# Performance work log

Measured on AMD Instinct MI355X. Metric: run time of the kernel, lower is better.

Reference implementation:

```python
import jax, jax.numpy as jnp
import numpy as np

RNN = 2048
NZ = 64
IN = 69  # 54 dofs + 15 actions


def gru_cell(x, h, w_ih, w_hh, b_ih, b_hh):
    gi = x @ w_ih.T + b_ih
    gh = h @ w_hh.T + b_hh
    i_r, i_z, i_n = jnp.split(gi, 3, axis=-1)
    h_r, h_z, h_n = jnp.split(gh, 3, axis=-1)
    r = jax.nn.sigmoid(i_r + h_r)
    z = jax.nn.sigmoid(i_z + h_z)
    n = jnp.tanh(i_n + r * h_n)
    return (1.0 - z) * n + z * h


def setup_inputs() -> dict:
    key = jax.random.key(0)
    ks = jax.random.split(key, 24)
    s = 0.02
    d = {
        'encoder_inputs': jax.random.normal(ks[0], (256, 49, IN), jnp.float32),
        'decoder_inputs': jax.random.normal(ks[1], (256, 25, IN), jnp.float32),
        'eps': jax.random.normal(ks[2], (256, NZ), jnp.float32),
        'fc0_w': jax.random.normal(ks[3], (RNN, 2 * IN), jnp.float32) * s,
        'fc0_b': jnp.zeros((RNN,), jnp.float32),
        'fc1_w': jax.random.normal(ks[4], (RNN, NZ + IN), jnp.float32) * s,
        'fc1_b': jnp.zeros((RNN,), jnp.float32),
        'fc2_w': jax.random.normal(ks[5], (IN, RNN), jnp.float32) * s,
        'fc2_b': jnp.zeros((IN,), jnp.float32),
        'mu_w': jax.random.normal(ks[6], (NZ, RNN), jnp.float32) * s,
        'mu_b': jnp.zeros((NZ,), jnp.float32),
        'sigma_w': jax.random.normal(ks[7], (NZ, RNN), jnp.float32) * s,
        'sigma_b': jnp.zeros((NZ,), jnp.float32),
        'c1_wih': jax.random.normal(ks[8], (3 * RNN, RNN), jnp.float32) * s,
        'c1_whh': jax.random.normal(ks[9], (3 * RNN, RNN), jnp.float32) * s,
        'c1_bih': jnp.zeros((3 * RNN,), jnp.float32),
        'c1_bhh': jnp.zeros((3 * RNN,), jnp.float32),
        'c2_wih': jax.random.normal(ks[10], (3 * RNN, IN), jnp.float32) * s,
        'c2_whh': jax.random.normal(ks[11], (3 * RNN, RNN), jnp.float32) * s,
        'c2_bih': jnp.zeros((3 * RNN,), jnp.float32),
        'c2_bhh': jnp.zeros((3 * RNN,), jnp.float32),
    }
    return d


def reference(encoder_inputs, decoder_inputs, eps, fc0_w, fc0_b, fc1_w, fc1_b, fc2_w, fc2_b,
              mu_w, mu_b, sigma_w, sigma_b, c1_wih, c1_whh, c1_bih, c1_bhh,
              c2_wih, c2_whh, c2_bih, c2_bhh):
    B = encoder_inputs.shape[0]
    enc_t = jnp.transpose(encoder_inputs, (1, 0, 2))  # [S-1, B, IN]
    dec_t = jnp.transpose(decoder_inputs, (1, 0, 2))  # [T, B, IN]
    # encoder step inputs: cat(enc[i], enc[i+1]); last step pairs with dec[0]
    nxt = jnp.concatenate([enc_t[1:], dec_t[:1]], axis=0)
    pairs = jnp.concatenate([enc_t, nxt], axis=-1)  # [S-1, B, 2*IN]
    x = pairs @ fc0_w.T + fc0_b  # fc0, [S-1, B, RNN]
    # precompute input-to-hidden GEMMs for all encoder steps
    gi_all = x @ c1_wih.T + c1_bih  # [S-1, B, 3*RNN]

    def enc_step(h, gi):
        gh = h @ c1_whh.T + c1_bhh
        i_r, i_z, i_n = jnp.split(gi, 3, axis=-1)
        h_r, h_z, h_n = jnp.split(gh, 3, axis=-1)
        r = jax.nn.sigmoid(i_r + h_r)
        z = jax.nn.sigmoid(i_z + h_z)
        n = jnp.tanh(i_n + r * h_n)
        return (1.0 - z) * n + z * h, None

    h0 = jnp.zeros((B, RNN), encoder_inputs.dtype)
    state, _ = jax.lax.scan(enc_step, h0, gi_all)

    z_mu = state @ mu_w.T + mu_b
    z_logvar = state @ sigma_w.T + sigma_b
    z = z_mu + eps * jnp.exp(0.5 * z_logvar)

    dec0 = dec_t[0]  # [B, IN]
    state = jnp.concatenate([z, dec0], axis=-1) @ fc1_w.T + fc1_b

    def dec_step(carry, _):
        h, inp = carry
        h = gru_cell(inp, h, c2_wih, c2_whh, c2_bih, c2_bhh)
        out = inp + (h @ fc2_w.T + fc2_b)  # residual feedback (eval: no dropout)
        return (h, out), out

    T = dec_t.shape[0]
    _, ys = jax.lax.scan(dec_step, (state, dec0), None, length=T)  # [T, B, IN]
    outputs = jnp.transpose(ys, (1, 0, 2))
    return outputs, z_mu, z_logvar
```

## Files before the change

kernel.cpp:

```cpp
#include <hip/hip_runtime.h>
#include <stdint.h>

#define B_    256
#define SE    49
#define TD    25
#define INDIM 69
#define RNN   2048
#define NZ    64
#define G3    6144

typedef __attribute__((ext_vector_type(8))) short short8_t;
typedef __attribute__((ext_vector_type(4))) float f32x4;
typedef unsigned short u16;

#define BARRIER() do { asm volatile("s_waitcnt lgkmcnt(0)" ::: "memory"); \
                       __builtin_amdgcn_s_barrier(); } while (0)

__device__ __forceinline__ u16 f2b(float f) {
  union { float f; unsigned u; } c; c.f = f;
  unsigned u = c.u;
  return (u16)((u + 0x7FFFu + ((u >> 16) & 1u)) >> 16);
}
__device__ __forceinline__ float sigm(float x) { return 1.f / (1.f + __expf(-x)); }
__device__ __forceinline__ short8_t ldbf(const u16* __restrict__ p, size_t off) {
  return *(const short8_t*)&p[off];
}

__device__ __forceinline__ int rmap(int R) {
  int bn = R / 96, rem = R % 96;
  int nw = rem / 48, g = (rem % 48) / 16, jj = rem % 16;
  return g * RNN + bn * 32 + nw * 16 + jj;
}

__global__ void k_reorder(const float* __restrict__ src, u16* __restrict__ dst, int K, int Kp) {
  int total = G3 * Kp;
  for (int i = blockIdx.x * blockDim.x + threadIdx.x; i < total; i += gridDim.x * blockDim.x) {
    int R = i / Kp, c = i % Kp;
    dst[i] = (c < K) ? f2b(src[(size_t)rmap(R) * K + c]) : (u16)0;
  }
}

__global__ void k_fc0T(const float* __restrict__ fc0w, const float* __restrict__ fc0b,
                       u16* __restrict__ dst) {
  int total = 256 * RNN;
  for (int i = blockIdx.x * blockDim.x + threadIdx.x; i < total; i += gridDim.x * blockDim.x) {
    int r = i >> 11, k = i & (RNN - 1);
    float v = 0.f;
    if (r < 2 * INDIM) v = fc0w[(size_t)k * (2 * INDIM) + r];
    else if (r == 2 * INDIM) v = fc0b[k];
    dst[i] = f2b(v);
  }
}

__global__ void k_fc2T(const float* __restrict__ fc2w, u16* __restrict__ dst) {
  int total = 96 * RNN;
  for (int i = blockIdx.x * blockDim.x + threadIdx.x; i < total; i += gridDim.x * blockDim.x) {
    int r = i >> 11, k = i & (RNN - 1);
    dst[i] = (r < INDIM) ? f2b(fc2w[(size_t)r * RNN + k]) : (u16)0;
  }
}

__global__ void k_pairs(const float* __restrict__ enc, const float* __restrict__ dec,
                        u16* __restrict__ pairs) {
  int total = SE * B_ * 256;
  for (int i = blockIdx.x * blockDim.x + threadIdx.x; i < total; i += gridDim.x * blockDim.x) {
    int c = i & 255, rb = i >> 8;
    int b = rb & 255, t = rb >> 8;
    float v = 0.f;
    if (c < INDIM) v = enc[((size_t)b * SE + t) * INDIM + c];
    else if (c < 2 * INDIM) {
      int cc = c - INDIM;
      v = (t < SE - 1) ? enc[((size_t)b * SE + t + 1) * INDIM + cc]
                       : dec[(size_t)b * TD * INDIM + cc];
    } else if (c == 2 * INDIM) v = 1.0f;
    pairs[i] = f2b(v);
  }
}

__global__ void k_msB(const float* __restrict__ muw, const float* __restrict__ sgw,
                      u16* __restrict__ dst) {
  int total = 128 * RNN;
  for (int i = blockIdx.x * blockDim.x + threadIdx.x; i < total; i += gridDim.x * blockDim.x) {
    int n = i >> 11, k = i & (RNN - 1);
    dst[i] = (n < NZ) ? f2b(muw[(size_t)n * RNN + k]) : f2b(sgw[(size_t)(n - NZ) * RNN + k]);
  }
}

__global__ void k_fc1B(const float* __restrict__ w, u16* __restrict__ dst) {
  int total = RNN * 192;
  for (int i = blockIdx.x * blockDim.x + threadIdx.x; i < total; i += gridDim.x * blockDim.x) {
    int n = i / 192, k = i % 192;
    dst[i] = (k < NZ + INDIM) ? f2b(w[(size_t)n * (NZ + INDIM) + k]) : (u16)0;
  }
}

__global__ void k_bias(const float* __restrict__ c1bih, const float* __restrict__ c1bhh,
                       const float* __restrict__ c2wih, const float* __restrict__ fc2b,
                       const float* __restrict__ c2bih, const float* __restrict__ c2bhh,
                       float* __restrict__ ebi, float* __restrict__ ebh,
                       float* __restrict__ dbi0, float* __restrict__ dbi1, float* __restrict__ dbh) {
  int R = blockIdx.x * blockDim.x + threadIdx.x;
  if (R >= G3) return;
  int orig = rmap(R);
  float k3 = 0.f;
  for (int o = 0; o < INDIM; ++o) k3 += c2wih[(size_t)orig * INDIM + o] * fc2b[o];
  ebi[R] = c1bih[orig];
  ebh[R] = c1bhh[orig];
  float d0 = c2bih[orig];
  dbi0[R] = d0;
  dbi1[R] = d0 + k3;
  dbh[R] = c2bhh[orig];
}

__global__ void k_init(float* __restrict__ hf, u16* __restrict__ hbf, float* __restrict__ fbuf,
                       float* __restrict__ omu, float* __restrict__ olv) {
  int i = blockIdx.x * blockDim.x + threadIdx.x;
  if (i < B_ * RNN) { hf[i] = 0.f; hbf[i] = 0; }
  if (i < 3 * B_ * 96) fbuf[i] = 0.f;
  if (i < B_ * NZ) { omu[i] = 0.f; olv[i] = 0.f; }
}

__global__ __launch_bounds__(256) void gemm_bt(
    const u16* __restrict__ A, const u16* __restrict__ W,
    u16* __restrict__ Cb, int N, int K)
{
  constexpr int BM = 128, BN = 128, BK = 64, LDK = BK + 8;
  __shared__ u16 sA[BM * LDK];
  __shared__ u16 sW[BN * LDK];
  const int ntn = N / BN;
  const int bm = blockIdx.x / ntn, bn = blockIdx.x % ntn;
  const int tid = threadIdx.x, lane = tid & 63, wave = tid >> 6;
  const int wr = wave >> 1, wc = wave & 1;
  f32x4 acc[4][4];
#pragma unroll
  for (int i = 0; i < 4; ++i)
#pragma unroll
    for (int j = 0; j < 4; ++j) acc[i][j] = (f32x4)(0.f);
  const int frow = lane & 15, fkq = (lane >> 4) * 8;
  for (int k0 = 0; k0 < K; k0 += BK) {
#pragma unroll
    for (int p = 0; p < 4; ++p) {
      int e = (p * 256 + tid) * 8, r = e / BK, c = e % BK;
      *(short8_t*)&sA[r * LDK + c] = *(const short8_t*)&A[(size_t)(bm * BM + r) * K + k0 + c];
    }
#pragma unroll
    for (int p = 0; p < 4; ++p) {
      int e = (p * 256 + tid) * 8, r = e / BK, c = e % BK;
      *(short8_t*)&sW[r * LDK + c] = *(const short8_t*)&W[(size_t)(bn * BN + r) * K + k0 + c];
    }
    __syncthreads();
#pragma unroll
    for (int kk = 0; kk < BK; kk += 32) {
      short8_t fa[4], fb[4];
#pragma unroll
      for (int m = 0; m < 4; ++m) fa[m] = *(const short8_t*)&sA[(wr * 64 + m * 16 + frow) * LDK + kk + fkq];
#pragma unroll
      for (int n = 0; n < 4; ++n) fb[n] = *(const short8_t*)&sW[(wc * 64 + n * 16 + frow) * LDK + kk + fkq];
#pragma unroll
      for (int m = 0; m < 4; ++m)
#pragma unroll
        for (int n = 0; n < 4; ++n)
          acc[m][n] = __builtin_amdgcn_mfma_f32_16x16x32_bf16(fa[m], fb[n], acc[m][n], 0, 0, 0);
    }
    __syncthreads();
  }
  const int crow = (lane >> 4) * 4, ccol = lane & 15;
#pragma unroll
  for (int n = 0; n < 4; ++n) {
    int col = bn * BN + wc * 64 + n * 16 + ccol;
#pragma unroll
    for (int m = 0; m < 4; ++m)
#pragma unroll
      for (int r = 0; r < 4; ++r) {
        int rowi = bm * BM + wr * 64 + m * 16 + crow + r;
        Cb[(size_t)rowi * N + col] = f2b(acc[m][n][r]);
      }
  }
}

struct Args {
  const u16 *pairs, *Wenc, *whh1, *whh2, *wih2, *fc2T;
  const u16 *msB, *fc1wB;
  const float *ebi, *ebh, *dbi0, *dbi1, *dbh;
  const float *eps, *dec, *fc1_b, *fc2_b, *mu_b, *sg_b;
  float* hf;
  u16*   hbf;
  float* fbuf;
  float* inp;
  u16*   inpbf;
  u16*   fc1xB;
  float *out, *out_mu, *out_lv;
};

__device__ __forceinline__ void compute_gi(const char* sA, const char* sW,
    f32x4 (&aR)[4], f32x4 (&aZ)[4], f32x4 (&aN)[4], int kg, int nw, int lane) {
#pragma unroll
  for (int s = 0; s < 2; ++s) {
    const int L = kg * 8 + s * 4 + (lane >> 4);
    short8_t fa[4], fb[3];
#pragma unroll
    for (int m = 0; m < 4; ++m) {
      int r = m * 16 + (lane & 15);
      fa[m] = *(const short8_t*)&sA[r * 512 + ((L ^ (r & 7)) * 16)];
    }
#pragma unroll
    for (int g = 0; g < 3; ++g) {
      int r = nw * 48 + g * 16 + (lane & 15);
      fb[g] = *(const short8_t*)&sW[r * 512 + ((L ^ (r & 7)) * 16)];
    }
#pragma unroll
    for (int m = 0; m < 4; ++m) {
      aR[m] = __builtin_amdgcn_mfma_f32_16x16x32_bf16(fa[m], fb[0], aR[m], 0, 0, 0);
      aZ[m] = __builtin_amdgcn_mfma_f32_16x16x32_bf16(fa[m], fb[1], aZ[m], 0, 0, 0);
      aN[m] = __builtin_amdgcn_mfma_f32_16x16x32_bf16(fa[m], fb[2], aN[m], 0, 0, 0);
    }
  }
}

__device__ __forceinline__ void compute_gh(const char* base,
    f32x4 (&aR)[4], f32x4 (&aZ)[4], f32x4 (&aN)[4], int kg, int nw, int lane) {
  const char* sA = base;
  const char* sW = base + 16384;
  const int L = kg * 4 + (lane >> 4);
  short8_t fa[4], fb[3];
#pragma unroll
  for (int m = 0; m < 4; ++m) {
    int r = m * 16 + (lane & 15);
    fa[m] = *(const short8_t*)&sA[r * 256 + ((L ^ (r & 15)) * 16)];
  }
#pragma unroll
  for (int g = 0; g < 3; ++g) {
    int r = nw * 48 + g * 16 + (lane & 15);
    fb[g] = *(const short8_t*)&sW[r * 256 + ((L ^ (r & 15)) * 16)];
  }
#pragma unroll
  for (int m = 0; m < 4; ++m) {
    aR[m] = __builtin_amdgcn_mfma_f32_16x16x32_bf16(fa[m], fb[0], aR[m], 0, 0, 0);
    aZ[m] = __builtin_amdgcn_mfma_f32_16x16x32_bf16(fa[m], fb[1], aZ[m], 0, 0, 0);
    aN[m] = __builtin_amdgcn_mfma_f32_16x16x32_bf16(fa[m], fb[2], aN[m], 0, 0, 0);
  }
}

__device__ __forceinline__ void reduce_and_gate(
    f32x4 (&aR)[4], f32x4 (&aZ)[4], f32x4 (&aNI)[4], f32x4 (&aNH)[4],
    char* smem, int tid, int bm, int bn,
    const float* __restrict__ bi, const float* __restrict__ bh,
    const float* __restrict__ hfold, float* __restrict__ hfnew, u16* __restrict__ hbnew) {
  const int lane = tid & 63, wid = tid >> 6;
  auto wr16 = [&](int slots, int w) {
#pragma unroll
    for (int m = 0; m < 4; ++m) {
      *(f32x4*)&smem[(((0 * 4 + m) * slots + w) * 64 + lane) * 16] = aR[m];
      *(f32x4*)&smem[(((1 * 4 + m) * slots + w) * 64 + lane) * 16] = aZ[m];
      *(f32x4*)&smem[(((2 * 4 + m) * slots + w) * 64 + lane) * 16] = aNI[m];
      *(f32x4*)&smem[(((3 * 4 + m) * slots + w) * 64 + lane) * 16] = aNH[m];
    }
  };
  auto add16 = [&](int slots, int w) {
#pragma unroll
    for (int m = 0; m < 4; ++m) {
      aR[m]  += *(const f32x4*)&smem[(((0 * 4 + m) * slots + w) * 64 + lane) * 16];
      aZ[m]  += *(const f32x4*)&smem[(((1 * 4 + m) * slots + w) * 64 + lane) * 16];
      aNI[m] += *(const f32x4*)&smem[(((2 * 4 + m) * slots + w) * 64 + lane) * 16];
      aNH[m] += *(const f32x4*)&smem[(((3 * 4 + m) * slots + w) * 64 + lane) * 16];
    }
  };
  __syncthreads();
  if (wid >= 4) wr16(4, wid - 4);
  __syncthreads();
  if (wid < 4) add16(4, wid);
  __syncthreads();
  if (wid == 2 || wid == 3) wr16(2, wid - 2);
  __syncthreads();
  if (wid < 2) {
    add16(2, wid);
    const int nw = wid, jj = lane & 15;
    const int Rb = bn * 96 + nw * 48;
    const float biR = bi[Rb + jj],      bhR = bh[Rb + jj];
    const float biZ = bi[Rb + 16 + jj], bhZ = bh[Rb + 16 + jj];
    const float biN = bi[Rb + 32 + jj], bhN = bh[Rb + 32 + jj];
    const int j = bn * 32 + nw * 16 + jj;
#pragma unroll
    for (int m = 0; m < 4; ++m)
#pragma unroll
      for (int q = 0; q < 4; ++q) {
        int b = bm * 64 + m * 16 + ((lane >> 4) << 2) + q;
        float r = sigm(aR[m][q] + biR + bhR);
        float z = sigm(aZ[m][q] + biZ + bhZ);
        float nn = 2.f * sigm(2.f * ((aNI[m][q] + biN) + r * (aNH[m][q] + bhN))) - 1.f;
        float hv = (1.f - z) * nn + z * hfold[(size_t)b * RNN + j];
        hfnew[(size_t)b * RNN + j] = hv;
        hbnew[(size_t)b * RNN + j] = f2b(hv);
      }
  }
}

__global__ __launch_bounds__(512, 1) void k_enc(Args a, int t) {
  __shared__ char smem[81920];
  const int tid = threadIdx.x, lane = tid & 63, wid = tid >> 6;
  const int kg = wid >> 1, nw = wid & 1;
  const int bm = blockIdx.x >> 6, bn = blockIdx.x & 63;
  const int rowA0 = bm * 64, rowW0 = bn * 96;
  const int pin = t & 1, pout = pin ^ 1;
  const u16* hin = a.hbf + (size_t)pin * B_ * RNN;
  const float* hfold = a.hf + (size_t)pin * B_ * RNN;
  float* hfnew = a.hf + (size_t)pout * B_ * RNN;
  u16* hbnew = a.hbf + (size_t)pout * B_ * RNN;
  const int sr32 = tid >> 5, sc32 = tid & 31;
  const int sr16 = tid >> 4, sc16 = tid & 15;

  f32x4 aR[4], aZ[4], aNI[4], aNH[4];
#pragma unroll
  for (int m = 0; m < 4; ++m) {
    aR[m] = (f32x4)(0.f); aZ[m] = (f32x4)(0.f);
    aNI[m] = (f32x4)(0.f); aNH[m] = (f32x4)(0.f);
  }

  auto issue_gh = [&](short8_t (&ra)[2], short8_t (&rw)[3], int k0) {
#pragma unroll
    for (int p = 0; p < 2; ++p) {
      int r = p * 32 + sr16;
      ra[p] = ldbf(hin, (size_t)(rowA0 + r) * RNN + k0 + sc16 * 8);
    }
#pragma unroll
    for (int p = 0; p < 3; ++p) {
      int r = p * 32 + sr16;
      rw[p] = ldbf(a.whh1, (size_t)(rowW0 + r) * RNN + k0 + sc16 * 8);
    }
  };
  auto write_gh = [&](char* base, short8_t (&ra)[2], short8_t (&rw)[3]) {
#pragma unroll
    for (int p = 0; p < 2; ++p) {
      int r = p * 32 + sr16;
      *(short8_t*)&base[r * 256 + ((sc16 ^ (r & 15)) * 16)] = ra[p];
    }
#pragma unroll
    for (int p = 0; p < 3; ++p) {
      int r = p * 32 + sr16;
      *(short8_t*)&(base + 16384)[r * 256 + ((sc16 ^ (r & 15)) * 16)] = rw[p];
    }
  };

  {
    const u16* P = a.pairs + (size_t)t * B_ * 256;
    short8_t ga[4], gw[6];
#pragma unroll
    for (int p = 0; p < 4; ++p) {
      int r = p * 16 + sr32;
      ga[p] = ldbf(P, (size_t)(rowA0 + r) * 256 + sc32 * 8);
    }
#pragma unroll
    for (int p = 0; p < 6; ++p) {
      int r = p * 16 + sr32;
      gw[p] = ldbf(a.Wenc, (size_t)(rowW0 + r) * 256 + sc32 * 8);
    }
#pragma unroll
    for (int p = 0; p < 4; ++p) {
      int r = p * 16 + sr32;
      *(short8_t*)&smem[r * 512 + ((sc32 ^ (r & 7)) * 16)] = ga[p];
    }
#pragma unroll
    for (int p = 0; p < 6; ++p) {
      int r = p * 16 + sr32;
      *(short8_t*)&smem[32768 + r * 512 + ((sc32 ^ (r & 7)) * 16)] = gw[p];
    }
  }
  short8_t rA0[2], rW0[3], rA1[2], rW1[3];
  issue_gh(rA0, rW0, 0);
  issue_gh(rA1, rW1, 128);
  BARRIER();
  compute_gi(smem, smem + 32768, aR, aZ, aNI, kg, nw, lane);
  BARRIER();
  write_gh(smem, rA0, rW0);
  issue_gh(rA0, rW0, 2 * 128);
  BARRIER();
#pragma unroll
  for (int i = 0; i < 16; ++i) {
    char* cb = (i & 1) ? smem + 40960 : smem;
    if (i + 1 <= 15) {
      char* nb = ((i + 1) & 1) ? smem + 40960 : smem;
      if ((i + 1) & 1) {
        write_gh(nb, rA1, rW1);
        if (i + 3 <= 15) issue_gh(rA1, rW1, (i + 3) * 128);
      } else {
        write_gh(nb, rA0, rW0);
        if (i + 3 <= 15) issue_gh(rA0, rW0, (i + 3) * 128);
      }
    }
    compute_gh(cb, aR, aZ, aNH, kg, nw, lane);
    if (i < 15) BARRIER();
  }
  reduce_and_gate(aR, aZ, aNI, aNH, smem, tid, bm, bn, a.ebi, a.ebh, hfold, hfnew, hbnew);
}

__global__ __launch_bounds__(512, 1) void k_dec(Args a, int t) {
  __shared__ char smem[81920];
  const int tid = threadIdx.x, lane = tid & 63, wid = tid >> 6;
  const int kg = wid >> 1, nw = wid & 1;
  const int bm = blockIdx.x >> 6, bn = blockIdx.x & 63;
  const int rowA0 = bm * 64, rowW0 = bn * 96;
  const int pin = t & 1, pout = pin ^ 1;
  const int irs = (t + 1) & 1, iws = t & 1;
  const int frd = (t + 2) % 3;
  const u16* hin = a.hbf + (size_t)pin * B_ * RNN;
  const float* hfold = a.hf + (size_t)pin * B_ * RNN;
  float* hfnew = a.hf + (size_t)pout * B_ * RNN;
  u16* hbnew = a.hbf + (size_t)pout * B_ * RNN;
  const int gtid = blockIdx.x * 512 + tid;
  const int sr32 = tid >> 5, sc32 = tid & 31;
  const int sr16 = tid >> 4, sc16 = tid & 15;
  const int fr = lane & 15, fq = (lane >> 4) << 3;

  if (t >= 1 && gtid < B_ * INDIM) {
    int b = gtid / INDIM, o = gtid % INDIM;
    float v = a.inp[(size_t)irs * B_ * INDIM + gtid] +
              a.fbuf[(size_t)frd * B_ * 96 + b * 96 + o] + a.fc2_b[o];
    a.out[((size_t)b * TD + (t - 1)) * INDIM + o] = v;
    a.inp[(size_t)iws * B_ * INDIM + gtid] = v;
    a.inpbf[(size_t)iws * B_ * 128 + b * 128 + o] = f2b(v);
  }
  if (gtid < B_ * 96)
    a.fbuf[(size_t)((t + 1) % 3) * B_ * 96 + gtid] = 0.f;

  f32x4 aR[4], aZ[4], aNI[4], aNH[4];
#pragma unroll
  for (int m = 0; m < 4; ++m) {
    aR[m] = (f32x4)(0.f); aZ[m] = (f32x4)(0.f);
    aNI[m] = (f32x4)(0.f); aNH[m] = (f32x4)(0.f);
  }

  auto issue_gh = [&](short8_t (&ra)[2], short8_t (&rw)[3], int k0) {
#pragma unroll
    for (int p = 0; p < 2; ++p) {
      int r = p * 32 + sr16;
      ra[p] = ldbf(hin, (size_t)(rowA0 + r) * RNN + k0 + sc16 * 8);
    }
#pragma unroll
    for (int p = 0; p < 3; ++p) {
      int r = p * 32 + sr16;
      rw[p] = ldbf(a.whh2, (size_t)(rowW0 + r) * RNN + k0 + sc16 * 8);
    }
  };
  auto write_gh = [&](char* base, short8_t (&ra)[2], short8_t (&rw)[3]) {
#pragma unroll
    for (int p = 0; p < 2; ++p) {
      int r = p * 32 + sr16;
      *(short8_t*)&base[r * 256 + ((sc16 ^ (r & 15)) * 16)] = ra[p];
    }
#pragma unroll
    for (int p = 0; p < 3; ++p) {
      int r = p * 32 + sr16;
      *(short8_t*)&(base + 16384)[r * 256 + ((sc16 ^ (r & 15)) * 16)] = rw[p];
    }
  };

  {
    const u16* inpA = a.inpbf + (size_t)irs * B_ * 128;
    const float* F = a.fbuf + (size_t)frd * B_ * 96;
    short8_t ga[4], gw[6];
#pragma unroll
    for (int p = 0; p < 4; ++p) {
      int r = p * 16 + sr32;
      if (sc32 < 16) {
        ga[p] = ldbf(inpA, (size_t)(rowA0 + r) * 128 + sc32 * 8);
      } else {
        short8_t v;
        int o0 = (sc32 - 16) * 8;
#pragma unroll
        for (int e = 0; e < 8; ++e) {
          int o = o0 + e;
          float fv = (o < 96) ? F[(size_t)(rowA0 + r) * 96 + o] : 0.f;
          v[e] = (short)f2b(fv);
        }
        ga[p] = v;
      }
    }
#pragma unroll
    for (int p = 0; p < 6; ++p) {
      int r = p * 16 + sr32;
      gw[p] = ldbf(a.wih2, (size_t)(rowW0 + r) * 128 + (sc32 & 15) * 8);
    }
#pragma unroll
    for (int p = 0; p < 4; ++p) {
      int r = p * 16 + sr32;
      *(short8_t*)&smem[r * 512 + ((sc32 ^ (r & 7)) * 16)] = ga[p];
    }
#pragma unroll
    for (int p = 0; p < 6; ++p) {
      int r = p * 16 + sr32;
      *(short8_t*)&smem[32768 + r * 512 + ((sc32 ^ (r & 7)) * 16)] = gw[p];
    }
  }
  short8_t rA0[2], rW0[3], rA1[2], rW1[3];
  issue_gh(rA0, rW0, 0);
  issue_gh(rA1, rW1, 128);
  BARRIER();
  compute_gi(smem, smem + 32768, aR, aZ, aNI, kg, nw, lane);
  BARRIER();
  write_gh(smem, rA0, rW0);
  issue_gh(rA0, rW0, 2 * 128);
  BARRIER();
#pragma unroll
  for (int i = 0; i < 16; ++i) {
    char* cb = (i & 1) ? smem + 40960 : smem;
    if (i + 1 <= 15) {
      char* nb = ((i + 1) & 1) ? smem + 40960 : smem;
      if ((i + 1) & 1) {
        write_gh(nb, rA1, rW1);
        if (i + 3 <= 15) issue_gh(rA1, rW1, (i + 3) * 128);
      } else {
        write_gh(nb, rA0, rW0);
        if (i + 3 <= 15) issue_gh(rA0, rW0, (i + 3) * 128);
      }
    }
    compute_gh(cb, aR, aZ, aNH, kg, nw, lane);
    if (i < 15) BARRIER();
  }
  reduce_and_gate(aR, aZ, aNI, aNH, smem, tid, bm, bn,
                  (t >= 1) ? a.dbi1 : a.dbi0, a.dbh, hfold, hfnew, hbnew);

  __syncthreads();
  if (wid < 4) {
    const int wr = wid >> 1, wc = wid & 1;
    const int kcol = bn * 32 + fq;
    short8_t fa[2], fb[3];
#pragma unroll
    for (int m = 0; m < 2; ++m)
      fa[m] = ldbf(hbnew, (size_t)(bm * 64 + wr * 32 + m * 16 + fr) * RNN + kcol);
#pragma unroll
    for (int n = 0; n < 3; ++n)
      fb[n] = ldbf(a.fc2T, (size_t)(wc * 48 + n * 16 + fr) * RNN + kcol);
    f32x4 accf[2][3];
#pragma unroll
    for (int m = 0; m < 2; ++m)
#pragma unroll
      for (int n = 0; n < 3; ++n) accf[m][n] = (f32x4)(0.f);
#pragma unroll
    for (int m = 0; m < 2; ++m)
#pragma unroll
      for (int n = 0; n < 3; ++n)
        accf[m][n] = __builtin_amdgcn_mfma_f32_16x16x32_bf16(fa[m], fb[n], accf[m][n], 0, 0, 0);
    float* fdst = a.fbuf + (size_t)(t % 3) * B_ * 96;
#pragma unroll
    for (int m = 0; m < 2; ++m)
#pragma unroll
      for (int n = 0; n < 3; ++n)
#pragma unroll
        for (int q = 0; q < 4; ++q) {
          int row = bm * 64 + wr * 32 + m * 16 + ((lane >> 4) << 2) + q;
          int col = wc * 48 + n * 16 + (lane & 15);
          atomicAdd(&fdst[row * 96 + col], accf[m][n][q]);
        }
  }
}

__global__ __launch_bounds__(256) void k_msm(Args a) {
  const int bm = blockIdx.x >> 3, kc = blockIdx.x & 7;
  const int lane = threadIdx.x & 63, wid = threadIdx.x >> 6;
  const int wr = wid >> 1, wc = wid & 1;
  const int fr = lane & 15, fq = (lane >> 4) << 3;
  const u16* h1 = a.hbf + (size_t)B_ * RNN;
  f32x4 acc[4][4];
#pragma unroll
  for (int m = 0; m < 4; ++m)
#pragma unroll
    for (int n = 0; n < 4; ++n) acc[m][n] = (f32x4)(0.f);
#pragma unroll
  for (int ks = 0; ks < 8; ++ks) {
    const int k = kc * 256 + ks * 32 + fq;
    short8_t fa[4], fb[4];
#pragma unroll
    for (int m = 0; m < 4; ++m)
      fa[m] = ldbf(h1, (size_t)(bm * 128 + wr * 64 + m * 16 + fr) * RNN + k);
#pragma unroll
    for (int n = 0; n < 4; ++n)
      fb[n] = ldbf(a.msB, (size_t)(wc * 64 + n * 16 + fr) * RNN + k);
#pragma unroll
    for (int m = 0; m < 4; ++m)
#pragma unroll
      for (int n = 0; n < 4; ++n)
        acc[m][n] = __builtin_amdgcn_mfma_f32_16x16x32_bf16(fa[m], fb[n], acc[m][n], 0, 0, 0);
  }
#pragma unroll
  for (int m = 0; m < 4; ++m)
#pragma unroll
    for (int n = 0; n < 4; ++n)
#pragma unroll
      for (int q = 0; q < 4; ++q) {
        int row = bm * 128 + wr * 64 + m * 16 + ((lane >> 4) << 2) + q;
        int col = wc * 64 + n * 16 + (lane & 15);
        if (col < NZ) atomicAdd(&a.out_mu[row * NZ + col], acc[m][n][q]);
        else          atomicAdd(&a.out_lv[row * NZ + col - NZ], acc[m][n][q]);
      }
}

__global__ void k_sample(Args a) {
  int gid = blockIdx.x * blockDim.x + threadIdx.x;
  if (gid < B_ * NZ) {
    int b = gid >> 6, n = gid & 63;
    float mu = a.out_mu[gid] + a.mu_b[n];
    float lv = a.out_lv[gid] + a.sg_b[n];
    a.out_mu[gid] = mu;
    a.out_lv[gid] = lv;
    a.fc1xB[b * 192 + n] = f2b(mu + a.eps[gid] * __expf(0.5f * lv));
  }
  if (gid < B_ * 128) {
    int b = gid >> 7, c = gid & 127;
    float v = (c < INDIM) ? a.dec[(size_t)b * TD * INDIM + c] : 0.f;
    u16 vb = f2b(v);
    a.inpbf[(size_t)b * 128 + c] = vb;
    a.inpbf[(size_t)B_ * 128 + b * 128 + c] = vb;
    if (c < INDIM) {
      a.inp[b * INDIM + c] = v;
      a.inp[B_ * INDIM + b * INDIM + c] = v;
      a.fc1xB[b * 192 + NZ + c] = f2b(v);
    }
  }
  if (gid < B_ * 192) {
    int c = gid % 192;
    if (c >= NZ + INDIM) a.fc1xB[gid] = 0;
  }
}

__global__ __launch_bounds__(256) void k_fc1m(Args a) {
  const int bm = blockIdx.x >> 4, bn = blockIdx.x & 15;
  const int lane = threadIdx.x & 63, wid = threadIdx.x >> 6;
  const int wr = wid >> 1, wc = wid & 1;
  const int fr = lane & 15, fq = (lane >> 4) << 3;
  f32x4 acc[4][4];
#pragma unroll
  for (int m = 0; m < 4; ++m)
#pragma unroll
    for (int n = 0; n < 4; ++n) acc[m][n] = (f32x4)(0.f);
#pragma unroll
  for (int ks = 0; ks < 6; ++ks) {
    const int k = ks * 32 + fq;
    short8_t fa[4], fb[4];
#pragma unroll
    for (int m = 0; m < 4; ++m)
      fa[m] = ldbf(a.fc1xB, (size_t)(bm * 128 + wr * 64 + m * 16 + fr) * 192 + k);
#pragma unroll
    for (int n = 0; n < 4; ++n)
      fb[n] = ldbf(a.fc1wB, (size_t)(bn * 128 + wc * 64 + n * 16 + fr) * 192 + k);
#pragma unroll
    for (int m = 0; m < 4; ++m)
#pragma unroll
      for (int n = 0; n < 4; ++n)
        acc[m][n] = __builtin_amdgcn_mfma_f32_16x16x32_bf16(fa[m], fb[n], acc[m][n], 0, 0, 0);
  }
#pragma unroll
  for (int n = 0; n < 4; ++n) {
    const int col = bn * 128 + wc * 64 + n * 16 + (lane & 15);
    const float bv = a.fc1_b[col];
#pragma unroll
    for (int m = 0; m < 4; ++m)
#pragma unroll
      for (int q = 0; q < 4; ++q) {
        int row = bm * 128 + wr * 64 + m * 16 + ((lane >> 4) << 2) + q;
        float v = acc[m][n][q] + bv;
        a.hf[(size_t)row * RNN + col] = v;
        a.hbf[(size_t)row * RNN + col] = f2b(v);
      }
  }
}

__global__ void k_tail(Args a) {
  int i = blockIdx.x * blockDim.x + threadIdx.x;
  if (i < B_ * INDIM) {
    int b = i / INDIM, o = i % INDIM;
    float v = a.inp[(size_t)(24 & 1) * B_ * INDIM + i] +
              a.fbuf[(size_t)(24 % 3) * B_ * 96 + b * 96 + o] + a.fc2_b[o];
    a.out[((size_t)b * TD + 24) * INDIM + o] = v;
  }
}

extern "C" void kernel_launch(void* const* d_in, const int* in_sizes, int n_in,
                              void* d_out, int out_size, void* d_ws, size_t ws_size,
                              hipStream_t stream)
{
  const float* enc    = (const float*)d_in[0];
  const float* dec    = (const float*)d_in[1];
  const float* eps    = (const float*)d_in[2];
  const float* fc0_w  = (const float*)d_in[3];
  const float* fc0_b  = (const float*)d_in[4];
  const float* fc1_w  = (const float*)d_in[5];
  const float* fc1_b  = (const float*)d_in[6];
  const float* fc2_w  = (const float*)d_in[7];
  const float* fc2_b  = (const float*)d_in[8];
  const float* mu_w   = (const float*)d_in[9];
  const float* mu_b   = (const float*)d_in[10];
  const float* sg_w   = (const float*)d_in[11];
  const float* sg_b   = (const float*)d_in[12];
  const float* c1_wih = (const float*)d_in[13];
  const float* c1_whh = (const float*)d_in[14];
  const float* c1_bih = (const float*)d_in[15];
  const float* c1_bhh = (const float*)d_in[16];
  const float* c2_wih = (const float*)d_in[17];
  const float* c2_whh = (const float*)d_in[18];
  const float* c2_bih = (const float*)d_in[19];
  const float* c2_bhh = (const float*)d_in[20];

  float* out_outputs = (float*)d_out;
  float* out_mu = out_outputs + (size_t)B_ * TD * INDIM;
  float* out_lv = out_mu + (size_t)B_ * NZ;

  char* ws = (char*)d_ws;
  size_t off = 0;
  auto alloc = [&](size_t bytes) -> void* {
    void* p = ws + off; off += (bytes + 255) & ~(size_t)255; return p;
  };

  u16* whh1_r = (u16*)alloc((size_t)G3 * RNN * 2);
  u16* whh2_r = (u16*)alloc((size_t)G3 * RNN * 2);
  u16* wih1_r = (u16*)alloc((size_t)G3 * RNN * 2);
  u16* wih2_r = (u16*)alloc((size_t)G3 * 128 * 2);
  u16* fc0T   = (u16*)alloc((size_t)256 * RNN * 2);
  u16* fc2T   = (u16*)alloc((size_t)96 * RNN * 2);
  u16* Wenc   = (u16*)alloc((size_t)G3 * 256 * 2);
  u16* pairs  = (u16*)alloc((size_t)SE * B_ * 256 * 2);
  u16* msB    = (u16*)alloc((size_t)128 * RNN * 2);
  u16* fc1wB  = (u16*)alloc((size_t)RNN * 192 * 2);
  float* hf   = (float*)alloc((size_t)2 * B_ * RNN * 4);
  u16* hbf    = (u16*)alloc((size_t)2 * B_ * RNN * 2);
  float* fbuf = (float*)alloc((size_t)3 * B_ * 96 * 4);
  float* inp  = (float*)alloc((size_t)2 * B_ * INDIM * 4);
  u16* inpbf  = (u16*)alloc((size_t)2 * B_ * 128 * 2);
  u16* fc1xB  = (u16*)alloc((size_t)B_ * 192 * 2);
  float* ebi  = (float*)alloc((size_t)G3 * 4);
  float* ebh  = (float*)alloc((size_t)G3 * 4);
  float* dbi0 = (float*)alloc((size_t)G3 * 4);
  float* dbi1 = (float*)alloc((size_t)G3 * 4);
  float* dbh  = (float*)alloc((size_t)G3 * 4);
  (void)ws_size; (void)in_sizes; (void)n_in; (void)out_size;

  k_reorder<<<4096, 256, 0, stream>>>(c1_whh, whh1_r, RNN, RNN);
  k_reorder<<<4096, 256, 0, stream>>>(c2_whh, whh2_r, RNN, RNN);
  k_reorder<<<4096, 256, 0, stream>>>(c1_wih, wih1_r, RNN, RNN);
  k_reorder<<<1024, 256, 0, stream>>>(c2_wih, wih2_r, INDIM, 128);
  k_fc0T<<<512, 256, 0, stream>>>(fc0_w, fc0_b, fc0T);
  k_fc2T<<<256, 256, 0, stream>>>(fc2_w, fc2T);
  k_pairs<<<2048, 256, 0, stream>>>(enc, dec, pairs);
  k_msB<<<256, 256, 0, stream>>>(mu_w, sg_w, msB);
  k_fc1B<<<256, 256, 0, stream>>>(fc1_w, fc1wB);
  k_bias<<<24, 256, 0, stream>>>(c1_bih, c1_bhh, c2_wih, fc2_b, c2_bih, c2_bhh,
                                 ebi, ebh, dbi0, dbi1, dbh);

  Args a;
  a.pairs = pairs; a.Wenc = Wenc; a.whh1 = whh1_r; a.whh2 = whh2_r;
  a.wih2 = wih2_r; a.fc2T = fc2T; a.msB = msB; a.fc1wB = fc1wB;
  a.ebi = ebi; a.ebh = ebh; a.dbi0 = dbi0; a.dbi1 = dbi1; a.dbh = dbh;
  a.eps = eps; a.dec = dec; a.fc1_b = fc1_b; a.fc2_b = fc2_b;
  a.mu_b = mu_b; a.sg_b = sg_b;
  a.hf = hf; a.hbf = hbf; a.fbuf = fbuf; a.inp = inp; a.inpbf = inpbf;
  a.fc1xB = fc1xB; a.out = out_outputs; a.out_mu = out_mu; a.out_lv = out_lv;

  k_init<<<2048, 256, 0, stream>>>(hf, hbf, fbuf, out_mu, out_lv);
  gemm_bt<<<(G3 / 128) * (256 / 128), 256, 0, stream>>>(wih1_r, fc0T, Wenc, 256, RNN);

  for (int t = 0; t < SE; ++t)
    k_enc<<<256, 512, 0, stream>>>(a, t);
  k_msm<<<16, 256, 0, stream>>>(a);
  k_sample<<<192, 256, 0, stream>>>(a);
  k_fc1m<<<32, 256, 0, stream>>>(a);
  for (int t = 0; t < TD; ++t)
    k_dec<<<256, 512, 0, stream>>>(a, t);
  k_tail<<<69, 256, 0, stream>>>(a);
}
```

Baseline: 1.435 ms.

## Fuse per-step GRU launches into persistent cooperative kernels with grid sync

Replaces the 49 encoder and 25 decoder per-timestep kernel launches with one cooperative kernel each. The kernel loops over timesteps and uses a cooperative-groups grid barrier between steps, falling back to per-step launches if the cooperative launch fails. This removes launch overhead and the kernel-boundary drain between dependent steps. In exchange it adds a grid-wide sync cost and relies on all 256 blocks being co-resident. The decoder also relies on memory ordering across the grid barrier for the fbuf atomics and the inp handoff.

```diff
diff --git a/kernel.cpp b/kernel.cpp
--- a/kernel.cpp
+++ b/kernel.cpp
@@ -1,5 +1,8 @@
 #include <hip/hip_runtime.h>
+#include <hip/hip_cooperative_groups.h>
 #include <stdint.h>
+
+namespace cg = cooperative_groups;
 
 #define B_    256
 #define SE    49
@@ -247,7 +250,7 @@
     const float* __restrict__ bi, const float* __restrict__ bh,
     const float* __restrict__ hfold, float* __restrict__ hfnew, u16* __restrict__ hbnew) {
   const int lane = tid & 63, wid = tid >> 6;
-  auto wr16 = [&](int slots, int w) {
+  auto wrp = [&](int slots, int w) {
 #pragma unroll
     for (int m = 0; m < 4; ++m) {
       *(f32x4*)&smem[(((0 * 4 + m) * slots + w) * 64 + lane) * 16] = aR[m];
@@ -256,7 +259,7 @@
       *(f32x4*)&smem[(((3 * 4 + m) * slots + w) * 64 + lane) * 16] = aNH[m];
     }
   };
-  auto add16 = [&](int slots, int w) {
+  auto addp = [&](int slots, int w) {
 #pragma unroll
     for (int m = 0; m < 4; ++m) {
       aR[m]  += *(const f32x4*)&smem[(((0 * 4 + m) * slots + w) * 64 + lane) * 16];
@@ -266,14 +269,14 @@
     }
   };
   __syncthreads();
-  if (wid >= 4) wr16(4, wid - 4);
+  if (wid >= 4) wrp(4, wid - 4);
   __syncthreads();
-  if (wid < 4) add16(4, wid);
+  if (wid < 4) addp(4, wid);
   __syncthreads();
-  if (wid == 2 || wid == 3) wr16(2, wid - 2);
+  if (wid == 2 || wid == 3) wrp(2, wid - 2);
   __syncthreads();
   if (wid < 2) {
-    add16(2, wid);
+    addp(2, wid);
     const int nw = wid, jj = lane & 15;
     const int Rb = bn * 96 + nw * 48;
     const float biR = bi[Rb + jj],      bhR = bh[Rb + jj];
@@ -295,262 +298,274 @@
   }
 }
 
-__global__ __launch_bounds__(512, 1) void k_enc(Args a, int t) {
+template<int COOP>
+__global__ __launch_bounds__(512, 1) void k_enc_run(Args a, int t0, int nsteps) {
   __shared__ char smem[81920];
   const int tid = threadIdx.x, lane = tid & 63, wid = tid >> 6;
   const int kg = wid >> 1, nw = wid & 1;
   const int bm = blockIdx.x >> 6, bn = blockIdx.x & 63;
   const int rowA0 = bm * 64, rowW0 = bn * 96;
-  const int pin = t & 1, pout = pin ^ 1;
-  const u16* hin = a.hbf + (size_t)pin * B_ * RNN;
-  const float* hfold = a.hf + (size_t)pin * B_ * RNN;
-  float* hfnew = a.hf + (size_t)pout * B_ * RNN;
-  u16* hbnew = a.hbf + (size_t)pout * B_ * RNN;
   const int sr32 = tid >> 5, sc32 = tid & 31;
   const int sr16 = tid >> 4, sc16 = tid & 15;
 
-  f32x4 aR[4], aZ[4], aNI[4], aNH[4];
-#pragma unroll
-  for (int m = 0; m < 4; ++m) {
-    aR[m] = (f32x4)(0.f); aZ[m] = (f32x4)(0.f);
-    aNI[m] = (f32x4)(0.f); aNH[m] = (f32x4)(0.f);
-  }
-
-  auto issue_gh = [&](short8_t (&ra)[2], short8_t (&rw)[3], int k0) {
-#pragma unroll
-    for (int p = 0; p < 2; ++p) {
-      int r = p * 32 + sr16;
-      ra[p] = ldbf(hin, (size_t)(rowA0 + r) * RNN + k0 + sc16 * 8);
-    }
-#pragma unroll
-    for (int p = 0; p < 3; ++p) {
-      int r = p * 32 + sr16;
-      rw[p] = ldbf(a.whh1, (size_t)(rowW0 + r) * RNN + k0 + sc16 * 8);
-    }
-  };
-  auto write_gh = [&](char* base, short8_t (&ra)[2], short8_t (&rw)[3]) {
-#pragma unroll
-    for (int p = 0; p < 2; ++p) {
-      int r = p * 32 + sr16;
-      *(short8_t*)&base[r * 256 + ((sc16 ^ (r & 15)) * 16)] = ra[p];
-    }
-#pragma unroll
-    for (int p = 0; p < 3; ++p) {
-      int r = p * 32 + sr16;
-      *(short8_t*)&(base + 16384)[r * 256 + ((sc16 ^ (r & 15)) * 16)] = rw[p];
-    }
-  };
-
-  {
-    const u16* P = a.pairs + (size_t)t * B_ * 256;
-    short8_t ga[4], gw[6];
-#pragma unroll
-    for (int p = 0; p < 4; ++p) {
-      int r = p * 16 + sr32;
-      ga[p] = ldbf(P, (size_t)(rowA0 + r) * 256 + sc32 * 8);
-    }
-#pragma unroll
-    for (int p = 0; p < 6; ++p) {
-      int r = p * 16 + sr32;
-      gw[p] = ldbf(a.Wenc, (size_t)(rowW0 + r) * 256 + sc32 * 8);
-    }
-#pragma unroll
-    for (int p = 0; p < 4; ++p) {
-      int r = p * 16 + sr32;
-      *(short8_t*)&smem[r * 512 + ((sc32 ^ (r & 7)) * 16)] = ga[p];
-    }
-#pragma unroll
-    for (int p = 0; p < 6; ++p) {
-      int r = p * 16 + sr32;
-      *(short8_t*)&smem[32768 + r * 512 + ((sc32 ^ (r & 7)) * 16)] = gw[p];
-    }
-  }
-  short8_t rA0[2], rW0[3], rA1[2], rW1[3];
-  issue_gh(rA0, rW0, 0);
-  issue_gh(rA1, rW1, 128);
-  BARRIER();
-  compute_gi(smem, smem + 32768, aR, aZ, aNI, kg, nw, lane);
-  BARRIER();
-  write_gh(smem, rA0, rW0);
-  issue_gh(rA0, rW0, 2 * 128);
-  BARRIER();
-#pragma unroll
-  for (int i = 0; i < 16; ++i) {
-    char* cb = (i & 1) ? smem + 40960 : smem;
-    if (i + 1 <= 15) {
-      char* nb = ((i + 1) & 1) ? smem + 40960 : smem;
-      if ((i + 1) & 1) {
-        write_gh(nb, rA1, rW1);
-        if (i + 3 <= 15) issue_gh(rA1, rW1, (i + 3) * 128);
-      } else {
-        write_gh(nb, rA0, rW0);
-        if (i + 3 <= 15) issue_gh(rA0, rW0, (i + 3) * 128);
-      }
-    }
-    compute_gh(cb, aR, aZ, aNH, kg, nw, lane);
-    if (i < 15) BARRIER();
-  }
-  reduce_and_gate(aR, aZ, aNI, aNH, smem, tid, bm, bn, a.ebi, a.ebh, hfold, hfnew, hbnew);
-}
-
-__global__ __launch_bounds__(512, 1) void k_dec(Args a, int t) {
+  for (int t = t0; t < t0 + nsteps; ++t) {
+    const int pin = t & 1, pout = pin ^ 1;
+    const u16* hin = a.hbf + (size_t)pin * B_ * RNN;
+    const float* hfold = a.hf + (size_t)pin * B_ * RNN;
+    float* hfnew = a.hf + (size_t)pout * B_ * RNN;
+    u16* hbnew = a.hbf + (size_t)pout * B_ * RNN;
+
+    f32x4 aR[4], aZ[4], aNI[4], aNH[4];
+#pragma unroll
+    for (int m = 0; m < 4; ++m) {
+      aR[m] = (f32x4)(0.f); aZ[m] = (f32x4)(0.f);
+      aNI[m] = (f32x4)(0.f); aNH[m] = (f32x4)(0.f);
+    }
+
+    auto issue_gh = [&](short8_t (&ra)[2], short8_t (&rw)[3], int k0) {
+#pragma unroll
+      for (int p = 0; p < 2; ++p) {
+        int r = p * 32 + sr16;
+        ra[p] = ldbf(hin, (size_t)(rowA0 + r) * RNN + k0 + sc16 * 8);
+      }
+#pragma unroll
+      for (int p = 0; p < 3; ++p) {
+        int r = p * 32 + sr16;
+        rw[p] = ldbf(a.whh1, (size_t)(rowW0 + r) * RNN + k0 + sc16 * 8);
+      }
+    };
+    auto write_gh = [&](char* base, short8_t (&ra)[2], short8_t (&rw)[3]) {
+#pragma unroll
+      for (int p = 0; p < 2; ++p) {
+        int r = p * 32 + sr16;
+        *(short8_t*)&base[r * 256 + ((sc16 ^ (r & 15)) * 16)] = ra[p];
+      }
+#pragma unroll
+      for (int p = 0; p < 3; ++p) {
+        int r = p * 32 + sr16;
+        *(short8_t*)&(base + 16384)[r * 256 + ((sc16 ^ (r & 15)) * 16)] = rw[p];
+      }
+    };
+
+    {
+      const u16* P = a.pairs + (size_t)t * B_ * 256;
+      short8_t ga[4], gw[6];
+#pragma unroll
+      for (int p = 0; p < 4; ++p) {
+        int r = p * 16 + sr32;
+        ga[p] = ldbf(P, (size_t)(rowA0 + r) * 256 + sc32 * 8);
+      }
+#pragma unroll
+      for (int p = 0; p < 6; ++p) {
+        int r = p * 16 + sr32;
+        gw[p] = ldbf(a.Wenc, (size_t)(rowW0 + r) * 256 + sc32 * 8);
+      }
+#pragma unroll
+      for (int p = 0; p < 4; ++p) {
+        int r = p * 16 + sr32;
+        *(short8_t*)&smem[r * 512 + ((sc32 ^ (r & 7)) * 16)] = ga[p];
+      }
+#pragma unroll
+      for (int p = 0; p < 6; ++p) {
+        int r = p * 16 + sr32;
+        *(short8_t*)&(smem + 32768)[r * 512 + ((sc32 ^ (r & 7)) * 16)] = gw[p];
+      }
+    }
+    short8_t rA0[2], rW0[3], rA1[2], rW1[3];
+    issue_gh(rA0, rW0, 0);
+    issue_gh(rA1, rW1, 128);
+    BARRIER();
+    compute_gi(smem, smem + 32768, aR, aZ, aNI, kg, nw, lane);
+    BARRIER();
+    write_gh(smem, rA0, rW0);
+    issue_gh(rA0, rW0, 2 * 128);
+    BARRIER();
+#pragma unroll
+    for (int i = 0; i < 16; ++i) {
+      char* cb = (i & 1) ? smem + 40960 : smem;
+      if (i + 1 <= 15) {
+        char* nb = ((i + 1) & 1) ? smem + 40960 : smem;
+        if ((i + 1) & 1) {
+          write_gh(nb, rA1, rW1);
+          if (i + 3 <= 15) issue_gh(rA1, rW1, (i + 3) * 128);
+        } else {
+          write_gh(nb, rA0, rW0);
+          if (i + 3 <= 15) issue_gh(rA0, rW0, (i + 3) * 128);
+        }
+      }
+      compute_gh(cb, aR, aZ, aNH, kg, nw, lane);
+      if (i < 15) BARRIER();
+    }
+    reduce_and_gate(aR, aZ, aNI, aNH, smem, tid, bm, bn, a.ebi, a.ebh, hfold, hfnew, hbnew);
+
+    if (COOP && t + 1 < t0 + nsteps) cg::this_grid().sync();
+  }
+}
+
+template<int COOP>
+__global__ __launch_bounds__(512, 1) void k_dec_run(Args a, int t0, int nsteps) {
   __shared__ char smem[81920];
   const int tid = threadIdx.x, lane = tid & 63, wid = tid >> 6;
   const int kg = wid >> 1, nw = wid & 1;
   const int bm = blockIdx.x >> 6, bn = blockIdx.x & 63;
   const int rowA0 = bm * 64, rowW0 = bn * 96;
-  const int pin = t & 1, pout = pin ^ 1;
-  const int irs = (t + 1) & 1, iws = t & 1;
-  const int frd = (t + 2) % 3;
-  const u16* hin = a.hbf + (size_t)pin * B_ * RNN;
-  const float* hfold = a.hf + (size_t)pin * B_ * RNN;
-  float* hfnew = a.hf + (size_t)pout * B_ * RNN;
-  u16* hbnew = a.hbf + (size_t)pout * B_ * RNN;
-  const int gtid = blockIdx.x * 512 + tid;
   const int sr32 = tid >> 5, sc32 = tid & 31;
   const int sr16 = tid >> 4, sc16 = tid & 15;
   const int fr = lane & 15, fq = (lane >> 4) << 3;
-
-  if (t >= 1 && gtid < B_ * INDIM) {
-    int b = gtid / INDIM, o = gtid % INDIM;
-    float v = a.inp[(size_t)irs * B_ * INDIM + gtid] +
-              a.fbuf[(size_t)frd * B_ * 96 + b * 96 + o] + a.fc2_b[o];
-    a.out[((size_t)b * TD + (t - 1)) * INDIM + o] = v;
-    a.inp[(size_t)iws * B_ * INDIM + gtid] = v;
-    a.inpbf[(size_t)iws * B_ * 128 + b * 128 + o] = f2b(v);
-  }
-  if (gtid < B_ * 96)
-    a.fbuf[(size_t)((t + 1) % 3) * B_ * 96 + gtid] = 0.f;
-
-  f32x4 aR[4], aZ[4], aNI[4], aNH[4];
-#pragma unroll
-  for (int m = 0; m < 4; ++m) {
-    aR[m] = (f32x4)(0.f); aZ[m] = (f32x4)(0.f);
-    aNI[m] = (f32x4)(0.f); aNH[m] = (f32x4)(0.f);
-  }
-
-  auto issue_gh = [&](short8_t (&ra)[2], short8_t (&rw)[3], int k0) {
-#pragma unroll
-    for (int p = 0; p < 2; ++p) {
-      int r = p * 32 + sr16;
-      ra[p] = ldbf(hin, (size_t)(rowA0 + r) * RNN + k0 + sc16 * 8);
-    }
-#pragma unroll
-    for (int p = 0; p < 3; ++p) {
-      int r = p * 32 + sr16;
-      rw[p] = ldbf(a.whh2, (size_t)(rowW0 + r) * RNN + k0 + sc16 * 8);
-    }
-  };
-  auto write_gh = [&](char* base, short8_t (&ra)[2], short8_t (&rw)[3]) {
-#pragma unroll
-    for (int p = 0; p < 2; ++p) {
-      int r = p * 32 + sr16;
-      *(short8_t*)&base[r * 256 + ((sc16 ^ (r & 15)) * 16)] = ra[p];
-    }
-#pragma unroll
-    for (int p = 0; p < 3; ++p) {
-      int r = p * 32 + sr16;
-      *(short8_t*)&(base + 16384)[r * 256 + ((sc16 ^ (r & 15)) * 16)] = rw[p];
-    }
-  };
-
-  {
-    const u16* inpA = a.inpbf + (size_t)irs * B_ * 128;
-    const float* F = a.fbuf + (size_t)frd * B_ * 96;
-    short8_t ga[4], gw[6];
-#pragma unroll
-    for (int p = 0; p < 4; ++p) {
-      int r = p * 16 + sr32;
-      if (sc32 < 16) {
-        ga[p] = ldbf(inpA, (size_t)(rowA0 + r) * 128 + sc32 * 8);
-      } else {
-        short8_t v;
-        int o0 = (sc32 - 16) * 8;
-#pragma unroll
-        for (int e = 0; e < 8; ++e) {
-          int o = o0 + e;
-          float fv = (o < 96) ? F[(size_t)(rowA0 + r) * 96 + o] : 0.f;
-          v[e] = (short)f2b(fv);
+  const int gtid = blockIdx.x * 512 + tid;
+
+  for (int t = t0; t < t0 + nsteps; ++t) {
+    const int pin = t & 1, pout = pin ^ 1;
+    const int irs = (t + 1) & 1, iws = t & 1;
+    const int frd = (t + 2) % 3;
+    const u16* hin = a.hbf + (size_t)pin * B_ * RNN;
+    const float* hfold = a.hf + (size_t)pin * B_ * RNN;
+    float* hfnew = a.hf + (size_t)pout * B_ * RNN;
+    u16* hbnew = a.hbf + (size_t)pout * B_ * RNN;
+
+    if (t >= 1 && gtid < B_ * INDIM) {
+      int b = gtid / INDIM, o = gtid % INDIM;
+      float v = a.inp[(size_t)irs * B_ * INDIM + gtid] +
+                a.fbuf[(size_t)frd * B_ * 96 + b * 96 + o] + a.fc2_b[o];
+      a.out[((size_t)b * TD + (t - 1)) * INDIM + o] = v;
+      a.inp[(size_t)iws * B_ * INDIM + gtid] = v;
+      a.inpbf[(size_t)iws * B_ * 128 + b * 128 + o] = f2b(v);
+    }
+    if (gtid < B_ * 96)
+      a.fbuf[(size_t)((t + 1) % 3) * B_ * 96 + gtid] = 0.f;
+
+    f32x4 aR[4], aZ[4], aNI[4], aNH[4];
+#pragma unroll
+    for (int m = 0; m < 4; ++m) {
+      aR[m] = (f32x4)(0.f); aZ[m] = (f32x4)(0.f);
+      aNI[m] = (f32x4)(0.f); aNH[m] = (f32x4)(0.f);
+    }
+
+    auto issue_gh = [&](short8_t (&ra)[2], short8_t (&rw)[3], int k0) {
+#pragma unroll
+      for (int p = 0; p < 2; ++p) {
+        int r = p * 32 + sr16;
+        ra[p] = ldbf(hin, (size_t)(rowA0 + r) * RNN + k0 + sc16 * 8);
+      }
+#pragma unroll
+      for (int p = 0; p < 3; ++p) {
+        int r = p * 32 + sr16;
+        rw[p] = ldbf(a.whh2, (size_t)(rowW0 + r) * RNN + k0 + sc16 * 8);
+      }
+    };
+    auto write_gh = [&](char* base, short8_t (&ra)[2], short8_t (&rw)[3]) {
+#pragma unroll
+      for (int p = 0; p < 2; ++p) {
+        int r = p * 32 + sr16;
+        *(short8_t*)&base[r * 256 + ((sc16 ^ (r & 15)) * 16)] = ra[p];
+      }
+#pragma unroll
+      for (int p = 0; p < 3; ++p) {
+        int r = p * 32 + sr16;
+        *(short8_t*)&(base + 16384)[r * 256 + ((sc16 ^ (r & 15)) * 16)] = rw[p];
+      }
+    };
+
+    {
+      const u16* inpA = a.inpbf + (size_t)irs * B_ * 128;
+      const float* F = a.fbuf + (size_t)frd * B_ * 96;
+      short8_t ga[4], gw[6];
+#pragma unroll
+      for (int p = 0; p < 4; ++p) {
+        int r = p * 16 + sr32;
+        if (sc32 < 16) {
+          ga[p] = ldbf(inpA, (size_t)(rowA0 + r) * 128 + sc32 * 8);
+        } else {
+          short8_t v;
+          int o0 = (sc32 - 16) * 8;
+#pragma unroll
+          for (int e = 0; e < 8; ++e) {
+            int o = o0 + e;
+            float fv = (o < 96) ? F[(size_t)(rowA0 + r) * 96 + o] : 0.f;
+            v[e] = (short)f2b(fv);
+          }
+          ga[p] = v;
         }
-        ga[p] = v;
-      }
-    }
-#pragma unroll
-    for (int p = 0; p < 6; ++p) {
-      int r = p * 16 + sr32;
-      gw[p] = ldbf(a.wih2, (size_t)(rowW0 + r) * 128 + (sc32 & 15) * 8);
-    }
-#pragma unroll
-    for (int p = 0; p < 4; ++p) {
-      int r = p * 16 + sr32;
-      *(short8_t*)&smem[r * 512 + ((sc32 ^ (r & 7)) * 16)] = ga[p];
-    }
-#pragma unroll
-    for (int p = 0; p < 6; ++p) {
-      int r = p * 16 + sr32;
-      *(short8_t*)&smem[32768 + r * 512 + ((sc32 ^ (r & 7)) * 16)] = gw[p];
-    }
-  }
-  short8_t rA0[2], rW0[3], rA1[2], rW1[3];
-  issue_gh(rA0, rW0, 0);
-  issue_gh(rA1, rW1, 128);
-  BARRIER();
-  compute_gi(smem, smem + 32768, aR, aZ, aNI, kg, nw, lane);
-  BARRIER();
-  write_gh(smem, rA0, rW0);
-  issue_gh(rA0, rW0, 2 * 128);
-  BARRIER();
-#pragma unroll
-  for (int i = 0; i < 16; ++i) {
-    char* cb = (i & 1) ? smem + 40960 : smem;
-    if (i + 1 <= 15) {
-      char* nb = ((i + 1) & 1) ? smem + 40960 : smem;
-      if ((i + 1) & 1) {
-        write_gh(nb, rA1, rW1);
-        if (i + 3 <= 15) issue_gh(rA1, rW1, (i + 3) * 128);
-      } else {
-        write_gh(nb, rA0, rW0);
-        if (i + 3 <= 15) issue_gh(rA0, rW0, (i + 3) * 128);
-      }
-    }
-    compute_gh(cb, aR, aZ, aNH, kg, nw, lane);
-    if (i < 15) BARRIER();
-  }
-  reduce_and_gate(aR, aZ, aNI, aNH, smem, tid, bm, bn,
-                  (t >= 1) ? a.dbi1 : a.dbi0, a.dbh, hfold, hfnew, hbnew);
-
-  __syncthreads();
-  if (wid < 4) {
-    const int wr = wid >> 1, wc = wid & 1;
-    const int kcol = bn * 32 + fq;
-    short8_t fa[2], fb[3];
-#pragma unroll
-    for (int m = 0; m < 2; ++m)
-      fa[m] = ldbf(hbnew, (size_t)(bm * 64 + wr * 32 + m * 16 + fr) * RNN + kcol);
-#pragma unroll
-    for (int n = 0; n < 3; ++n)
-      fb[n] = ldbf(a.fc2T, (size_t)(wc * 48 + n * 16 + fr) * RNN + kcol);
-    f32x4 accf[2][3];
-#pragma unroll
-    for (int m = 0; m < 2; ++m)
-#pragma unroll
-      for (int n = 0; n < 3; ++n) accf[m][n] = (f32x4)(0.f);
-#pragma unroll
-    for (int m = 0; m < 2; ++m)
+      }
+#pragma unroll
+      for (int p = 0; p < 6; ++p) {
+        int r = p * 16 + sr32;
+        gw[p] = ldbf(a.wih2, (size_t)(rowW0 + r) * 128 + (sc32 & 15) * 8);
+      }
+#pragma unroll
+      for (int p = 0; p < 4; ++p) {
+        int r = p * 16 + sr32;
+        *(short8_t*)&smem[r * 512 + ((sc32 ^ (r & 7)) * 16)] = ga[p];
+      }
+#pragma unroll
+      for (int p = 0; p < 6; ++p) {
+        int r = p * 16 + sr32;
+        *(short8_t*)&(smem + 32768)[r * 512 + ((sc32 ^ (r & 7)) * 16)] = gw[p];
+      }
+    }
+    short8_t rA0[2], rW0[3], rA1[2], rW1[3];
+    issue_gh(rA0, rW0, 0);
+    issue_gh(rA1, rW1, 128);
+    BARRIER();
+    compute_gi(smem, smem + 32768, aR, aZ, aNI, kg, nw, lane);
+    BARRIER();
+    write_gh(smem, rA0, rW0);
+    issue_gh(rA0, rW0, 2 * 128);
+    BARRIER();
+#pragma unroll
+    for (int i = 0; i < 16; ++i) {
+      char* cb = (i & 1) ? smem + 40960 : smem;
+      if (i + 1 <= 15) {
+        char* nb = ((i + 1) & 1) ? smem + 40960 : smem;
+        if ((i + 1) & 1) {
+          write_gh(nb, rA1, rW1);
+          if (i + 3 <= 15) issue_gh(rA1, rW1, (i + 3) * 128);
+        } else {
+          write_gh(nb, rA0, rW0);
+          if (i + 3 <= 15) issue_gh(rA0, rW0, (i + 3) * 128);
+        }
+      }
+      compute_gh(cb, aR, aZ, aNH, kg, nw, lane);
+      if (i < 15) BARRIER();
+    }
+    reduce_and_gate(aR, aZ, aNI, aNH, smem, tid, bm, bn,
+                    (t >= 1) ? a.dbi1 : a.dbi0, a.dbh, hfold, hfnew, hbnew);
+
+    __syncthreads();
+    if (wid < 4) {
+      const int wr = wid >> 1, wc = wid & 1;
+      const int kcol = bn * 32 + fq;
+      short8_t fa[2], fb[3];
+#pragma unroll
+      for (int m = 0; m < 2; ++m)
+        fa[m] = ldbf(hbnew, (size_t)(bm * 64 + wr * 32 + m * 16 + fr) * RNN + kcol);
 #pragma unroll
       for (int n = 0; n < 3; ++n)
-        accf[m][n] = __builtin_amdgcn_mfma_f32_16x16x32_bf16(fa[m], fb[n], accf[m][n], 0, 0, 0);
-    float* fdst = a.fbuf + (size_t)(t % 3) * B_ * 96;
-#pragma unroll
-    for (int m = 0; m < 2; ++m)
-#pragma unroll
-      for (int n = 0; n < 3; ++n)
-#pragma unroll
-        for (int q = 0; q < 4; ++q) {
-          int row = bm * 64 + wr * 32 + m * 16 + ((lane >> 4) << 2) + q;
-          int col = wc * 48 + n * 16 + (lane & 15);
-          atomicAdd(&fdst[row * 96 + col], accf[m][n][q]);
-        }
+        fb[n] = ldbf(a.fc2T, (size_t)(wc * 48 + n * 16 + fr) * RNN + kcol);
+      f32x4 accf[2][3];
+#pragma unroll
+      for (int m = 0; m < 2; ++m)
+#pragma unroll
+        for (int n = 0; n < 3; ++n) accf[m][n] = (f32x4)(0.f);
+#pragma unroll
+      for (int m = 0; m < 2; ++m)
+#pragma unroll
+        for (int n = 0; n < 3; ++n)
+          accf[m][n] = __builtin_amdgcn_mfma_f32_16x16x32_bf16(fa[m], fb[n], accf[m][n], 0, 0, 0);
+      float* fdst = a.fbuf + (size_t)(t % 3) * B_ * 96;
+#pragma unroll
+      for (int m = 0; m < 2; ++m)
+#pragma unroll
+        for (int n = 0; n < 3; ++n)
+#pragma unroll
+          for (int q = 0; q < 4; ++q) {
+            int row = bm * 64 + wr * 32 + m * 16 + ((lane >> 4) << 2) + q;
+            int col = wc * 48 + n * 16 + (lane & 15);
+            atomicAdd(&fdst[row * 96 + col], accf[m][n][q]);
+          }
+    }
+
+    if (COOP && t + 1 < t0 + nsteps) cg::this_grid().sync();
   }
 }
 
@@ -757,12 +772,31 @@
   k_init<<<2048, 256, 0, stream>>>(hf, hbf, fbuf, out_mu, out_lv);
   gemm_bt<<<(G3 / 128) * (256 / 128), 256, 0, stream>>>(wih1_r, fc0T, Wenc, 256, RNN);
 
-  for (int t = 0; t < SE; ++t)
-    k_enc<<<256, 512, 0, stream>>>(a, t);
+  {
+    int t0 = 0, ns = SE;
+    void* params[3] = { (void*)&a, (void*)&t0, (void*)&ns };
+    hipError_t e = hipLaunchCooperativeKernel((const void*)k_enc_run<1>,
+                                              dim3(256), dim3(512), params, 0, stream);
+    if (e != hipSuccess) {
+      for (int t = 0; t < SE; ++t)
+        k_enc_run<0><<<256, 512, 0, stream>>>(a, t, 1);
+    }
+  }
+
   k_msm<<<16, 256, 0, stream>>>(a);
   k_sample<<<192, 256, 0, stream>>>(a);
   k_fc1m<<<32, 256, 0, stream>>>(a);
-  for (int t = 0; t < TD; ++t)
-    k_dec<<<256, 512, 0, stream>>>(a, t);
+
+  {
+    int t0 = 0, ns = TD;
+    void* params[3] = { (void*)&a, (void*)&t0, (void*)&ns };
+    hipError_t e = hipLaunchCooperativeKernel((const void*)k_dec_run<1>,
+                                              dim3(256), dim3(512), params, 0, stream);
+    if (e != hipSuccess) {
+      for (int t = 0; t < TD; ++t)
+        k_dec_run<0><<<256, 512, 0, stream>>>(a, t, 1);
+    }
+  }
+
   k_tail<<<69, 256, 0, stream>>>(a);
 }
```

After: 3.611 ms. 2.52x slower.
